# Performance work log

Measured on AMD Instinct MI355X. Metric: run time of the kernel, lower is better.

The kernel has to match this reference:

```python
import jax, jax.numpy as jnp
import numpy as np

EPS = 1e-5
GRID = (16, 16)
BLOCK = (16, 16)


def _ln(x):
    # LayerNorm over (C, H, W) per sample, affine = identity (fresh nn.LayerNorm each call)
    m = jnp.mean(x, axis=(1, 2, 3), keepdims=True)
    v = jnp.mean(jnp.square(x - m), axis=(1, 2, 3), keepdims=True)
    return (x - m) / jnp.sqrt(v + EPS)


def _gelu(x):
    return jax.nn.gelu(x, approximate=False)  # torch F.gelu default = exact erf


def _block(x, fh, fw):
    # NCHW -> [N, C, gh*gw, fh*fw]
    n, c, h, w = x.shape
    gh, gw = h // fh, w // fw
    return x.reshape(n, c, gh, fh, gw, fw).transpose(0, 1, 2, 4, 3, 5).reshape(n, c, gh * gw, fh * fw)


def _unblock(x, gh, gw, fh, fw):
    n, c, _, _ = x.shape
    return x.reshape(n, c, gh, gw, fh, fw).transpose(0, 1, 2, 4, 3, 5).reshape(n, c, gh * fh, gw * fw)


def _gating(x, w1, b1, w2, b2, w3, b3, w4, b4):
    # GetSpatialGatingWeights
    n, c, h, w = x.shape
    x = _ln(x)
    x = jnp.einsum('nchw,cd->ndhw', x, w1) + b1[None, :, None, None]  # C -> 2C
    x = _gelu(x)
    u, v = jnp.split(x, 2, axis=1)
    # grid MLP on u: mix across gh*gw grid positions
    gh, gw = GRID
    fh, fw = h // gh, w // gw
    u = _block(u, fh, fw)                                             # [n,c,G,P]
    u = jnp.einsum('ncgp,gd->ncdp', u, w2) + b2[None, None, :, None]
    u = _unblock(u, gh, gw, fh, fw)
    # block MLP on v: mix across fh*fw positions inside each block
    fh, fw = BLOCK
    gh, gw = h // fh, w // fw
    v = _block(v, fh, fw)
    v = jnp.einsum('ncgp,pd->ncgd', v, w3) + b3
    v = _unblock(v, gh, gw, fh, fw)
    x = jnp.concatenate([u, v], axis=1)
    return jnp.einsum('nchw,cd->ndhw', x, w4) + b4[None, :, None, None]  # 2C -> C


def _chan_lin(x, w, b):
    return jnp.einsum('nchw,cd->ndhw', x, w) + b[None, :, None, None]


def setup_inputs() -> dict:
    key = jax.random.key(0)
    ks = list(jax.random.split(key, 40))
    k = iter(ks)

    def rn(shape, s=0.02):
        return jax.random.normal(next(k), shape, dtype=jnp.float32) * s

    N, Cx, Cy, F, H, W = 8, 128, 256, 128, 128, 128
    G = GRID[0] * GRID[1]    # 256
    B = BLOCK[0] * BLOCK[1]  # 256
    inp = {
        'x': jax.random.normal(next(k), (N, Cx, H, W), dtype=jnp.float32),
        'y': jax.random.normal(next(k), (N, Cy, H // 2, W // 2), dtype=jnp.float32),
        'wt': rn((Cy, F, 2, 2)), 'bt': rn((F,)),
        'wc1': rn((Cx, F)), 'bc1': rn((F,)),
        'wc2': rn((F, F)), 'bc2': rn((F,)),
        'wl1': rn((F, F)), 'bl1': rn((F,)),
        'wl2': rn((F, F)), 'bl2': rn((F,)),
        'wl3': rn((F, F)), 'bl3': rn((F,)),
        'wl4': rn((F, F)), 'bl4': rn((F,)),
    }
    for p in ('g1', 'g2'):
        inp[p + '_w1'] = rn((F, 2 * F)); inp[p + '_b1'] = rn((2 * F,))
        inp[p + '_w2'] = rn((G, G));     inp[p + '_b2'] = rn((G,))
        inp[p + '_w3'] = rn((B, B));     inp[p + '_b3'] = rn((B,))
        inp[p + '_w4'] = rn((2 * F, F)); inp[p + '_b4'] = rn((F,))
    return inp


def reference(x, y, wt, bt, wc1, bc1, wc2, bc2, wl1, bl1, wl2, bl2, wl3, bl3, wl4, bl4,
              g1_w1, g1_b1, g1_w2, g1_b2, g1_w3, g1_b3, g1_w4, g1_b4,
              g2_w1, g2_b1, g2_w2, g2_b2, g2_w3, g2_b3, g2_w4, g2_b4):
    # ConvT_up: kernel=2, stride=2 (non-overlapping) + ReLU
    n, cy, hy, wy = y.shape
    fo = wt.shape[1]
    y = jnp.einsum('nchw,cokl->nohkwl', y, wt).reshape(n, fo, 2 * hy, 2 * wy) + bt[None, :, None, None]
    y = jax.nn.relu(y)
    # Conv1x1 (+ReLU) projections
    x = jax.nn.relu(_chan_lin(x, wc1, bc1))
    y = jax.nn.relu(_chan_lin(y, wc2, bc2))
    shortcut_x, shortcut_y = x, y
    # x branch
    x = _gelu(_chan_lin(_ln(x), wl1, bl1))
    gx = _gating(x, g1_w1, g1_b1, g1_w2, g1_b2, g1_w3, g1_b3, g1_w4, g1_b4)
    # y branch
    y = _gelu(_chan_lin(_ln(y), wl2, bl2))
    gy = _gating(y, g2_w1, g2_b1, g2_w2, g2_b2, g2_w3, g2_b3, g2_w4, g2_b4)
    # cross gating + residuals (dropout p=0.0 -> identity)
    y = _chan_lin(y * gx, wl3, bl3) + shortcut_y
    x = _chan_lin(x * gy, wl4, bl4) + y + shortcut_x
    return x, y
```

## Files before the change

### kernel.cpp

```cpp
#include <hip/hip_runtime.h>
#include <hip/hip_bf16.h>


typedef unsigned short u16;
typedef __bf16 bf16x8 __attribute__((ext_vector_type(8)));
typedef u16    u16x8  __attribute__((ext_vector_type(8)));
typedef u16    u16x4  __attribute__((ext_vector_type(4)));
typedef float  f32x4  __attribute__((ext_vector_type(4)));

__device__ __forceinline__ float bf2f(u16 u) {
  union { float f; unsigned int i; } v; v.i = ((unsigned int)u) << 16; return v.f;
}
__device__ __forceinline__ u16 f2bf(float f) {
  union { float f; unsigned int i; } v; v.f = f;
  unsigned int x = v.i;
  return (u16)((x + 0x7fffu + ((x >> 16) & 1u)) >> 16);
}
__device__ __forceinline__ f32x4 mfma16(u16x8 a, u16x8 b, f32x4 c) {
  return __builtin_amdgcn_mfma_f32_16x16x32_bf16(
      __builtin_bit_cast(bf16x8, a), __builtin_bit_cast(bf16x8, b), c, 0, 0, 0);
}
__device__ __forceinline__ float gelu_erf(float v) {
  const float z = v * (-2.3022586f - 0.10294276f * v * v);
  return __fdividef(v, 1.f + exp2f(z));
}

__global__ __launch_bounds__(256) void prep_k(
    const float* __restrict__ wc1f, const float* __restrict__ wc2f,
    const float* __restrict__ wl1f, const float* __restrict__ wl2f,
    const float* __restrict__ wl3f, const float* __restrict__ wl4f,
    const float* __restrict__ g1w1, const float* __restrict__ g2w1,
    const float* __restrict__ g1w4, const float* __restrict__ g2w4,
    const float* __restrict__ g1w2, const float* __restrict__ g2w2,
    const float* __restrict__ g1w3, const float* __restrict__ g2w3,
    const float* __restrict__ wtf,
    u16* __restrict__ wb, float* __restrict__ cs, float* __restrict__ ps) {
  const int b = blockIdx.x, t = threadIdx.x;
  if (b < 384) {
    const float* src = b < 64 ? wc1f : b < 128 ? wc2f : b < 192 ? wl1f
                     : b < 256 ? wl2f : b < 320 ? wl3f : wl4f;
    const int w = b >> 6;
    const int i = ((b & 63) << 8) + t;
    const int d = i >> 7, c = i & 127;
    wb[w * 16384 + i] = f2bf(src[c * 128 + d]);
  } else if (b < 640) {
    const float* src = b < 512 ? g1w1 : g2w1;
    const int base = b < 512 ? 98304 : 131072;
    const int i = (((b - (b < 512 ? 384 : 512)) << 8) + t);
    const int d = i >> 7, c = i & 127;
    wb[base + i] = f2bf(src[c * 256 + d]);
  } else if (b < 896) {
    const float* src = b < 768 ? g1w4 : g2w4;
    const int base = b < 768 ? 163840 : 196608;
    const int i = (((b - (b < 768 ? 640 : 768)) << 8) + t);
    const int d = i >> 8, c = i & 255;
    wb[base + i] = f2bf(src[c * 128 + d]);
  } else if (b < 1920) {
    const int w = (b - 896) >> 8;
    const float* src = w == 0 ? g1w2 : w == 1 ? g2w2 : w == 2 ? g1w3 : g2w3;
    const int base = 229376 + w * 65536;
    const int i = (((b - 896) & 255) << 8) + t;
    const int d = i >> 8, g = i & 255;
    wb[base + i] = f2bf(src[g * 256 + d]);
  } else if (b < 2432) {
    const int i = ((b - 1920) << 8) + t;
    const int c = i & 255, r = i >> 8, o = r & 127, kl = r >> 7;
    wb[491520 + i] = f2bf(wtf[(c * 128 + o) * 4 + kl]);
  } else if (b < 2436) {
    const int w = b - 2432;
    const float* src = w == 0 ? wl1f : w == 1 ? wl2f : w == 2 ? g1w1 : g2w1;
    const int cout = w < 2 ? 128 : 256;
    if (t < cout) {
      float s = 0.f;
      for (int c = 0; c < 128; ++c) s += bf2f(f2bf(src[c * cout + t]));
      cs[w * 256 + t] = s;
    }
  } else {
    if (t < 64) ps[t] = 0.f;
  }
}

__global__ __launch_bounds__(256, 2) void gemmYX_k(
    const float* __restrict__ Y, const float* __restrict__ X,
    const u16* __restrict__ Wtb, const float* __restrict__ bt,
    const u16* __restrict__ Wc2, const float* __restrict__ bc2,
    const u16* __restrict__ Wc1, const float* __restrict__ bc1,
    u16* __restrict__ oy, u16* __restrict__ ox, float* __restrict__ ps) {
  __shared__ u16 sm[25088];
  __shared__ float red[8];
  const int tid = threadIdx.x;
  const int wid = tid >> 6, lane = tid & 63, fr = lane & 15, fg = lane >> 4;

  if (blockIdx.x < 512) {
    u16* As = sm;
    u16* Cs = sm + 16384;
    float* pso = ps + 16;
    const int m0 = blockIdx.x * 64;
    const int ns = m0 >> 12, pb = m0 & 4095;
    const int tokg = (wid & 1) * 32;
    const int chg  = (wid >> 1) * 64;
    const int xorl = (fr & 7) << 4;

#pragma unroll
    for (int it = 0; it < 16; ++it) {
      const int idx = it * 256 + tid;
      const int c = idx & 255, t4 = idx >> 8;
      const f32x4 v = *(const f32x4*)(Y + (((size_t)(ns * 256 + c)) << 12) + pb + t4 * 4);
#pragma unroll
      for (int r = 0; r < 4; ++r) {
        const int tok = t4 * 4 + r;
        const int byte = (tok * 512 + c * 2) ^ ((tok & 7) << 4);
        *(u16*)((char*)As + byte) = f2bf(v[r]);
      }
    }
    __syncthreads();

    float s1 = 0.f, s2 = 0.f;
    for (int kl = 0; kl < 4; ++kl) {
      if (kl) __syncthreads();
      f32x4 acc1[2][4] = {};
      {
        const u16* Brow = Wtb + (size_t)(kl * 128 + chg + fr) * 256;
#pragma unroll
        for (int ks = 0; ks < 8; ++ks) {
          const int kb = ks * 32 + fg * 8;
          u16x8 a_[2], b_[4];
#pragma unroll
          for (int i = 0; i < 2; ++i) {
            const int tok = tokg + i * 16 + fr;
            const int byte = (tok * 512 + kb * 2) ^ xorl;
            a_[i] = *(const u16x8*)((const char*)As + byte);
          }
#pragma unroll
          for (int j = 0; j < 4; ++j)
            b_[j] = *(const u16x8*)(Brow + (size_t)j * 16 * 256 + kb);
#pragma unroll
          for (int i = 0; i < 2; ++i)
#pragma unroll
            for (int j = 0; j < 4; ++j) acc1[i][j] = mfma16(b_[j], a_[i], acc1[i][j]);
        }
      }
#pragma unroll
      for (int i = 0; i < 2; ++i) {
        const int tok = tokg + i * 16 + fr;
#pragma unroll
        for (int j = 0; j < 4; ++j) {
          const int o0 = chg + j * 16 + fg * 4;
          const f32x4 bz = *(const f32x4*)(bt + o0);
          u16x4 sv;
#pragma unroll
          for (int r = 0; r < 4; ++r) sv[r] = f2bf(fmaxf(acc1[i][j][r] + bz[r], 0.f));
          *(u16x4*)(Cs + tok * 136 + o0) = sv;
        }
      }
      __syncthreads();
      f32x4 acc2[2][4] = {};
      {
        const u16* Brow = Wc2 + (size_t)(chg + fr) * 128;
#pragma unroll
        for (int ks = 0; ks < 4; ++ks) {
          const int kb = ks * 32 + fg * 8;
          u16x8 a_[2], b_[4];
#pragma unroll
          for (int i = 0; i < 2; ++i)
            a_[i] = *(const u16x8*)(Cs + (tokg + i * 16 + fr) * 136 + kb);
#pragma unroll
          for (int j = 0; j < 4; ++j)
            b_[j] = *(const u16x8*)(Brow + (size_t)j * 16 * 128 + kb);
#pragma unroll
          for (int i = 0; i < 2; ++i)
#pragma unroll
            for (int j = 0; j < 4; ++j) acc2[i][j] = mfma16(b_[j], a_[i], acc2[i][j]);
        }
      }
#pragma unroll
      for (int i = 0; i < 2; ++i) {
        const int ytok = m0 + tokg + i * 16 + fr;
        const int hy = (ytok >> 6) & 63, wy = ytok & 63;
        const int opix = ((ns * 128 + 2 * hy + (kl >> 1)) << 7) + 2 * wy + (kl & 1);
#pragma unroll
        for (int j = 0; j < 4; ++j) {
          const int ch0 = chg + j * 16 + fg * 4;
          const f32x4 bz = *(const f32x4*)(bc2 + ch0);
          u16x4 sv;
#pragma unroll
          for (int r = 0; r < 4; ++r) {
            float v = fmaxf(acc2[i][j][r] + bz[r], 0.f);
            s1 += v; s2 += v * v;
            sv[r] = f2bf(v);
          }
          *(u16x4*)(oy + (size_t)opix * 128 + ch0) = sv;
        }
      }
    }
#pragma unroll
    for (int off = 32; off > 0; off >>= 1) {
      s1 += __shfl_down(s1, off); s2 += __shfl_down(s2, off);
    }
    if (lane == 0) { red[wid] = s1; red[4 + wid] = s2; }
    __syncthreads();
    if (tid == 0)  atomicAdd(&pso[2 * ns],     red[0] + red[1] + red[2] + red[3]);
    if (tid == 64) atomicAdd(&pso[2 * ns + 1], red[4] + red[5] + red[6] + red[7]);
  } else {
    u16* As = sm;
    float* pso = ps;
    const int m0 = (blockIdx.x - 512) * 128;
    const int ns = m0 >> 14, pb = m0 & 16383;
    const int wmt = (wid & 1) * 64, wnc = (wid >> 1) * 64;

#pragma unroll
    for (int it = 0; it < 16; ++it) {
      const int idx = it * 256 + tid;
      const int c = idx & 127, t4 = idx >> 7;
      const f32x4 v = *(const f32x4*)(X + (((size_t)(ns * 128 + c)) << 14) + pb + t4 * 4);
#pragma unroll
      for (int r = 0; r < 4; ++r) As[(t4 * 4 + r) * 136 + c] = f2bf(v[r]);
    }
    __syncthreads();

    f32x4 acc[4][4] = {};
    const u16* Brow = Wc1 + (size_t)(wnc + fr) * 128;
    u16x8 a[4][4];
#pragma unroll
    for (int ks = 0; ks < 4; ++ks) {
      const int kb = ks * 32 + fg * 8;
#pragma unroll
      for (int i = 0; i < 4; ++i)
        a[ks][i] = *(const u16x8*)(As + (wmt + i * 16 + fr) * 136 + kb);
    }
#pragma unroll
    for (int ks = 0; ks < 4; ++ks) {
      const int kb = ks * 32 + fg * 8;
      u16x8 b_[4];
#pragma unroll
      for (int j = 0; j < 4; ++j)
        b_[j] = *(const u16x8*)(Brow + (size_t)j * 16 * 128 + kb);
#pragma unroll
      for (int i = 0; i < 4; ++i)
#pragma unroll
        for (int j = 0; j < 4; ++j) acc[i][j] = mfma16(b_[j], a[ks][i], acc[i][j]);
    }

    float s1 = 0.f, s2 = 0.f;
#pragma unroll
    for (int i = 0; i < 4; ++i) {
      const int token = m0 + wmt + i * 16 + fr;
#pragma unroll
      for (int j = 0; j < 4; ++j) {
        const int ch0 = wnc + j * 16 + fg * 4;
        const f32x4 bz = *(const f32x4*)(bc1 + ch0);
        f32x4 v = acc[i][j];
        u16x4 sv;
#pragma unroll
        for (int r = 0; r < 4; ++r) {
          v[r] = fmaxf(v[r] + bz[r], 0.f);
          s1 += v[r]; s2 += v[r] * v[r];
          sv[r] = f2bf(v[r]);
        }
        *(u16x4*)(ox + (size_t)token * 128 + ch0) = sv;
      }
    }
#pragma unroll
    for (int off = 32; off > 0; off >>= 1) {
      s1 += __shfl_down(s1, off); s2 += __shfl_down(s2, off);
    }
    if (lane == 0) { red[wid] = s1; red[4 + wid] = s2; }
    __syncthreads();
    if (tid == 0)  atomicAdd(&pso[2 * ns],     red[0] + red[1] + red[2] + red[3]);
    if (tid == 64) atomicAdd(&pso[2 * ns + 1], red[4] + red[5] + red[6] + red[7]);
  }
}

__global__ __launch_bounds__(256, 2) void gemm4d_k(
    const u16* __restrict__ Ay, const u16* __restrict__ Ax,
    const u16* __restrict__ Wty, const u16* __restrict__ Wtx,
    const float* __restrict__ by, const float* __restrict__ bx,
    float* __restrict__ ps,
    const float* __restrict__ csy, const float* __restrict__ csx,
    u16* __restrict__ oy, u16* __restrict__ ox) {
  __shared__ float red[8];
  const int br = blockIdx.y;
  const u16* A1 = br ? Ax : Ay;
  const u16* Wt = br ? Wtx : Wty;
  const float* bias = br ? bx : by;
  const float* pst = ps + (br ? 0 : 16);
  float* pso = ps + (br ? 32 : 48);
  const float* cs = br ? csx : csy;
  u16* out = br ? ox : oy;

  const int tid = threadIdx.x;
  const int m0 = blockIdx.x * 128;
  const int wid = tid >> 6, lane = tid & 63, fr = lane & 15, fg = lane >> 4;
  const int wmt = (wid & 1) * 64, wnc = (wid >> 1) * 64;

  f32x4 acc[4][4] = {};
  const u16* Arow = A1 + (size_t)(m0 + wmt + fr) * 128;
  const u16* Brow = Wt + (size_t)(wnc + fr) * 128;

  u16x8 a[4][4];
#pragma unroll
  for (int ks = 0; ks < 4; ++ks) {
    const int kb = ks * 32 + fg * 8;
#pragma unroll
    for (int i = 0; i < 4; ++i)
      a[ks][i] = *(const u16x8*)(Arow + (size_t)i * 16 * 128 + kb);
  }
#pragma unroll
  for (int ks = 0; ks < 4; ++ks) {
    const int kb = ks * 32 + fg * 8;
    u16x8 b_[4];
#pragma unroll
    for (int j = 0; j < 4; ++j)
      b_[j] = *(const u16x8*)(Brow + (size_t)j * 16 * 128 + kb);
#pragma unroll
    for (int i = 0; i < 4; ++i)
#pragma unroll
      for (int j = 0; j < 4; ++j) acc[i][j] = mfma16(b_[j], a[ks][i], acc[i][j]);
  }

  const int s = m0 >> 14;
  const float inv_n = 1.f / 2097152.f;
  const float mean = pst[2 * s] * inv_n;
  const float var = pst[2 * s + 1] * inv_n - mean * mean;
  const float alpha = rsqrtf(var + 1e-5f);
  const float beta = -mean * alpha;

  float s1 = 0.f, s2 = 0.f;
#pragma unroll
  for (int i = 0; i < 4; ++i) {
    const int token = m0 + wmt + i * 16 + fr;
#pragma unroll
    for (int j = 0; j < 4; ++j) {
      const int ch0 = wnc + j * 16 + fg * 4;
      const f32x4 bz = *(const f32x4*)(bias + ch0);
      const f32x4 csv = *(const f32x4*)(cs + ch0);
      f32x4 v = acc[i][j];
      u16x4 sv;
#pragma unroll
      for (int r = 0; r < 4; ++r) {
        v[r] = v[r] * alpha + beta * csv[r] + bz[r];
        v[r] = gelu_erf(v[r]);
        s1 += v[r]; s2 += v[r] * v[r];
        sv[r] = f2bf(v[r]);
      }
      *(u16x4*)(out + (size_t)token * 128 + ch0) = sv;
    }
  }
#pragma unroll
  for (int off = 32; off > 0; off >>= 1) {
    s1 += __shfl_down(s1, off); s2 += __shfl_down(s2, off);
  }
  if (lane == 0) { red[wid] = s1; red[4 + wid] = s2; }
  __syncthreads();
  if (tid == 0)  atomicAdd(&pso[2 * s],     red[0] + red[1] + red[2] + red[3]);
  if (tid == 64) atomicAdd(&pso[2 * s + 1], red[4] + red[5] + red[6] + red[7]);
}

template <int MODE>
__global__ __launch_bounds__(512, 2) void mlp3c_k(
    const u16* __restrict__ a1y, const u16* __restrict__ a1x,
    const u16* __restrict__ w1y, const u16* __restrict__ w1x,
    const float* __restrict__ b1y, const float* __restrict__ b1x,
    const float* __restrict__ ps,
    const float* __restrict__ csy, const float* __restrict__ csx,
    const u16* __restrict__ w2y, const u16* __restrict__ w2x,
    const float* __restrict__ b2y, const float* __restrict__ b2x,
    const u16* __restrict__ w4y, const u16* __restrict__ w4x,
    const float* __restrict__ b4y, const float* __restrict__ b4x,
    u16* __restrict__ goy, u16* __restrict__ gox) {
  __shared__ u16 Ts[32768];
  const int br = blockIdx.z;
  const u16* y1 = br ? a1x : a1y;
  const u16* mulp = br ? a1y : a1x;
  const u16* w1b = br ? w1x : w1y;
  const float* b1 = br ? b1x : b1y;
  const float* pst = ps + (br ? 32 : 48);
  const float* csb = br ? csx : csy;
  const u16* w2b = br ? w2x : w2y;
  const float* b2 = br ? b2x : b2y;
  const u16* w4b = br ? w4x : w4y;
  const float* b4 = br ? b4x : b4y;
  u16* gout = br ? gox : goy;

  const int q2 = blockIdx.x, ns = blockIdx.y;
  const int tid = threadIdx.x;
  constexpr int coff = MODE ? 128 : 0;
  const int wid = tid >> 6, lane = tid & 63, fr = lane & 15, fg = lane >> 4;
  const int xorl = (fr & 7) << 4;

  int pbase, prow, pcol;
  if constexpr (MODE == 0) {
    pbase = ns * 16384 + (q2 >> 3) * 128 + (q2 & 7);
    prow = 1024; pcol = 8;
  } else {
    pbase = ns * 16384 + (q2 >> 3) * 2048 + (q2 & 7) * 16;
    prow = 128; pcol = 1;
  }
  auto pix = [&](int q) { return pbase + (q >> 4) * prow + (q & 15) * pcol; };

  {
    const int wgt = (wid >> 1) * 64;
    const int wc  = (wid & 1) * 64;
    const float inv_n = 1.f / 2097152.f;
    const float mean = pst[2 * ns] * inv_n;
    const float var = pst[2 * ns + 1] * inv_n - mean * mean;
    const float alpha = rsqrtf(var + 1e-5f);
    const float beta = -mean * alpha;

    f32x4 acc[4][4] = {};
    const u16* ar[4];
#pragma unroll
    for (int i = 0; i < 4; ++i)
      ar[i] = y1 + (size_t)pix(wgt + i * 16 + fr) * 128;
    const u16* br_ = w1b + (size_t)(coff + wc + fr) * 128;

    u16x8 a[4][4];
#pragma unroll
    for (int ks = 0; ks < 4; ++ks) {
      const int kb = ks * 32 + fg * 8;
#pragma unroll
      for (int i = 0; i < 4; ++i) a[ks][i] = *(const u16x8*)(ar[i] + kb);
    }
#pragma unroll
    for (int ks = 0; ks < 4; ++ks) {
      const int kb = ks * 32 + fg * 8;
      u16x8 b_[4];
#pragma unroll
      for (int j = 0; j < 4; ++j)
        b_[j] = *(const u16x8*)(br_ + (size_t)j * 16 * 128 + kb);
#pragma unroll
      for (int i = 0; i < 4; ++i)
#pragma unroll
        for (int j = 0; j < 4; ++j) acc[i][j] = mfma16(a[ks][i], b_[j], acc[i][j]);
    }
#pragma unroll
    for (int j = 0; j < 4; ++j) {
      const int c = wc + j * 16 + fr;
      const float cv = csb[coff + c];
      const float bz = b1[coff + c];
#pragma unroll
      for (int i = 0; i < 4; ++i) {
        const int g0 = wgt + i * 16 + fg * 4;
        u16x4 sv;
#pragma unroll
        for (int r = 0; r < 4; ++r)
          sv[r] = f2bf(gelu_erf(acc[i][j][r] * alpha + beta * cv + bz));
        const int byte = (c * 512 + g0 * 2) ^ xorl;
        *(u16x4*)((char*)Ts + byte) = sv;
      }
    }
  }
  __syncthreads();

  f32x4 accB[4][4];
  const int wcs = (wid >> 2) * 64;
  const int wds = (wid & 3) * 64;
  {
#pragma unroll
    for (int i = 0; i < 4; ++i)
#pragma unroll
      for (int j = 0; j < 4; ++j) accB[i][j] = f32x4{0.f, 0.f, 0.f, 0.f};
    const u16* br_ = w2b + (size_t)(wds + fr) * 256;
#pragma unroll
    for (int h = 0; h < 2; ++h) {
      u16x8 a[4][4];
#pragma unroll
      for (int ks = 0; ks < 4; ++ks) {
        const int kb = (h * 4 + ks) * 32 + fg * 8;
#pragma unroll
        for (int i = 0; i < 4; ++i) {
          const int c = wcs + i * 16 + fr;
          const int byte = (c * 512 + kb * 2) ^ xorl;
          a[ks][i] = *(const u16x8*)((const char*)Ts + byte);
        }
      }
#pragma unroll
      for (int ks = 0; ks < 4; ++ks) {
        const int kb = (h * 4 + ks) * 32 + fg * 8;
        u16x8 b_[4];
#pragma unroll
        for (int j = 0; j < 4; ++j)
          b_[j] = *(const u16x8*)(br_ + (size_t)j * 16 * 256 + kb);
#pragma unroll
        for (int i = 0; i < 4; ++i)
#pragma unroll
          for (int j = 0; j < 4; ++j) accB[i][j] = mfma16(a[ks][i], b_[j], accB[i][j]);
      }
    }
  }
  __syncthreads();

#pragma unroll
  for (int j = 0; j < 4; ++j) {
    const int d = wds + j * 16 + fr;
    const float bz = b2[d];
    const int dx = (d & 7) << 4;
#pragma unroll
    for (int i = 0; i < 4; ++i) {
      const int c0 = wcs + i * 16 + fg * 4;
      u16x4 sv;
#pragma unroll
      for (int r = 0; r < 4; ++r) sv[r] = f2bf(accB[i][j][r] + bz);
      const int byte = (d * 256 + c0 * 2) ^ dx;
      *(u16x4*)((char*)Ts + byte) = sv;
    }
  }
  __syncthreads();

  {
    const int wp = (wid >> 1) * 64;
    const int wo = (wid & 1) * 64;
    f32x4 accC[4][4] = {};
    const u16* br_ = w4b + (size_t)(wo + fr) * 256 + coff;
#pragma unroll
    for (int ks = 0; ks < 4; ++ks) {
      const int kb = ks * 32 + fg * 8;
      u16x8 a_[4], b_[4];
#pragma unroll
      for (int i = 0; i < 4; ++i) {
        const int dp = wp + i * 16 + fr;
        const int byte = (dp * 256 + kb * 2) ^ ((dp & 7) << 4);
        a_[i] = *(const u16x8*)((const char*)Ts + byte);
      }
#pragma unroll
      for (int j = 0; j < 4; ++j)
        b_[j] = *(const u16x8*)(br_ + (size_t)j * 16 * 256 + kb);
#pragma unroll
      for (int i = 0; i < 4; ++i)
#pragma unroll
        for (int j = 0; j < 4; ++j) accC[i][j] = mfma16(b_[j], a_[i], accC[i][j]);
    }
#pragma unroll
    for (int i = 0; i < 4; ++i) {
      const size_t pg = (size_t)pix(wp + i * 16 + fr) * 128;
#pragma unroll
      for (int j = 0; j < 4; ++j) {
        const int o0 = wo + j * 16 + fg * 4;
        f32x4 v = accC[i][j];
        u16x4 sv;
        if constexpr (MODE == 0) {
          const f32x4 bz = *(const f32x4*)(b4 + o0);
#pragma unroll
          for (int r = 0; r < 4; ++r) sv[r] = f2bf(v[r] + bz[r]);
        } else {
          const u16x4 pv = *(const u16x4*)(gout + pg + o0);
          const u16x4 mv = *(const u16x4*)(mulp + pg + o0);
#pragma unroll
          for (int r = 0; r < 4; ++r)
            sv[r] = f2bf((v[r] + bf2f(pv[r])) * bf2f(mv[r]));
        }
        *(u16x4*)(gout + pg + o0) = sv;
      }
    }
  }
}

__global__ __launch_bounds__(256, 2) void dual5_k(
    const u16* __restrict__ y1g, const u16* __restrict__ x1g,
    const u16* __restrict__ w3b, const u16* __restrict__ w4b,
    const float* __restrict__ b3, const float* __restrict__ b4,
    const u16* __restrict__ y0, const u16* __restrict__ x0,
    float* __restrict__ outy, float* __restrict__ outx) {
  const int tid = threadIdx.x;
  const int m0 = blockIdx.x * 128;
  const int wid = tid >> 6, lane = tid & 63, fr = lane & 15, fg = lane >> 4;
  const int wmt = (wid & 1) * 64, wnc = (wid >> 1) * 64;

  f32x4 acc[4][4] = {};
  u16x4 y9[4][4];

  {
    const u16* Arow = y1g + (size_t)(m0 + wmt + fr) * 128;
    const u16* Brow = w3b + (size_t)(wnc + fr) * 128;
    u16x8 a[4][4];
#pragma unroll
    for (int ks = 0; ks < 4; ++ks) {
      const int kb = ks * 32 + fg * 8;
#pragma unroll
      for (int i = 0; i < 4; ++i)
        a[ks][i] = *(const u16x8*)(Arow + (size_t)i * 16 * 128 + kb);
    }
#pragma unroll
    for (int ks = 0; ks < 4; ++ks) {
      const int kb = ks * 32 + fg * 8;
      u16x8 b_[4];
#pragma unroll
      for (int j = 0; j < 4; ++j) b_[j] = *(const u16x8*)(Brow + (size_t)j * 16 * 128 + kb);
#pragma unroll
      for (int i = 0; i < 4; ++i)
#pragma unroll
        for (int j = 0; j < 4; ++j) acc[i][j] = mfma16(b_[j], a[ks][i], acc[i][j]);
    }
  }
  {
    u16x4 scv[4][4];
#pragma unroll
    for (int i = 0; i < 4; ++i) {
      const int token = m0 + wmt + i * 16 + fr;
#pragma unroll
      for (int j = 0; j < 4; ++j)
        scv[i][j] = *(const u16x4*)(y0 + (size_t)token * 128 + wnc + j * 16 + fg * 4);
    }
#pragma unroll
    for (int i = 0; i < 4; ++i) {
      const int token = m0 + wmt + i * 16 + fr;
      const int ns = token >> 14, p = token & 16383;
#pragma unroll
      for (int j = 0; j < 4; ++j) {
        const int ch0 = wnc + j * 16 + fg * 4;
        const f32x4 bz = *(const f32x4*)(b3 + ch0);
        f32x4 v = acc[i][j];
#pragma unroll
        for (int r = 0; r < 4; ++r) {
          v[r] += bz[r] + bf2f(scv[i][j][r]);
          outy[((size_t)(ns * 128 + ch0 + r) << 14) + p] = v[r];
          y9[i][j][r] = f2bf(v[r]);
        }
        acc[i][j] = f32x4{0.f, 0.f, 0.f, 0.f};
      }
    }
  }
  {
    const u16* Arow = x1g + (size_t)(m0 + wmt + fr) * 128;
    const u16* Brow = w4b + (size_t)(wnc + fr) * 128;
    u16x8 a[4][4];
#pragma unroll
    for (int ks = 0; ks < 4; ++ks) {
      const int kb = ks * 32 + fg * 8;
#pragma unroll
      for (int i = 0; i < 4; ++i)
        a[ks][i] = *(const u16x8*)(Arow + (size_t)i * 16 * 128 + kb);
    }
#pragma unroll
    for (int ks = 0; ks < 4; ++ks) {
      const int kb = ks * 32 + fg * 8;
      u16x8 b_[4];
#pragma unroll
      for (int j = 0; j < 4; ++j) b_[j] = *(const u16x8*)(Brow + (size_t)j * 16 * 128 + kb);
#pragma unroll
      for (int i = 0; i < 4; ++i)
#pragma unroll
        for (int j = 0; j < 4; ++j) acc[i][j] = mfma16(b_[j], a[ks][i], acc[i][j]);
    }
  }
  {
    u16x4 scv[4][4];
#pragma unroll
    for (int i = 0; i < 4; ++i) {
      const int token = m0 + wmt + i * 16 + fr;
#pragma unroll
      for (int j = 0; j < 4; ++j)
        scv[i][j] = *(const u16x4*)(x0 + (size_t)token * 128 + wnc + j * 16 + fg * 4);
    }
#pragma unroll
    for (int i = 0; i < 4; ++i) {
      const int token = m0 + wmt + i * 16 + fr;
      const int ns = token >> 14, p = token & 16383;
#pragma unroll
      for (int j = 0; j < 4; ++j) {
        const int ch0 = wnc + j * 16 + fg * 4;
        const f32x4 bz = *(const f32x4*)(b4 + ch0);
        f32x4 v = acc[i][j];
#pragma unroll
        for (int r = 0; r < 4; ++r) {
          v[r] += bz[r] + bf2f(y9[i][j][r]) + bf2f(scv[i][j][r]);
          outx[((size_t)(ns * 128 + ch0 + r) << 14) + p] = v[r];
        }
      }
    }
  }
}

extern "C" void kernel_launch(void* const* d_in, const int* in_sizes, int n_in,
                              void* d_out, int out_size, void* d_ws, size_t ws_size,
                              hipStream_t stream) {
  (void)in_sizes; (void)n_in; (void)out_size; (void)ws_size;
  const float* xf   = (const float*)d_in[0];
  const float* yf   = (const float*)d_in[1];
  const float* wtf  = (const float*)d_in[2];
  const float* btf  = (const float*)d_in[3];
  const float* wc1f = (const float*)d_in[4];
  const float* bc1f = (const float*)d_in[5];
  const float* wc2f = (const float*)d_in[6];
  const float* bc2f = (const float*)d_in[7];
  const float* wl1f = (const float*)d_in[8];
  const float* bl1f = (const float*)d_in[9];
  const float* wl2f = (const float*)d_in[10];
  const float* bl2f = (const float*)d_in[11];
  const float* wl3f = (const float*)d_in[12];
  const float* bl3f = (const float*)d_in[13];
  const float* wl4f = (const float*)d_in[14];
  const float* bl4f = (const float*)d_in[15];
  const float* g1w1 = (const float*)d_in[16];
  const float* g1b1 = (const float*)d_in[17];
  const float* g1w2 = (const float*)d_in[18];
  const float* g1b2 = (const float*)d_in[19];
  const float* g1w3 = (const float*)d_in[20];
  const float* g1b3 = (const float*)d_in[21];
  const float* g1w4 = (const float*)d_in[22];
  const float* g1b4 = (const float*)d_in[23];
  const float* g2w1 = (const float*)d_in[24];
  const float* g2b1 = (const float*)d_in[25];
  const float* g2w2 = (const float*)d_in[26];
  const float* g2b2 = (const float*)d_in[27];
  const float* g2w3 = (const float*)d_in[28];
  const float* g2b3 = (const float*)d_in[29];
  const float* g2w4 = (const float*)d_in[30];
  const float* g2b4 = (const float*)d_in[31];

  constexpr int T16 = 16777216;
  u16* WS  = (u16*)d_ws;
  u16* x0b = WS;
  u16* x1b = WS + (size_t)T16;
  u16* y0b = WS + (size_t)2 * T16;
  u16* y1b = WS + (size_t)3 * T16;
  u16* gyb = WS + (size_t)4 * T16;
  u16* gxb = WS + (size_t)5 * T16;
  float* fb = (float*)(WS + (size_t)6 * T16);
  float* cs = fb;
  float* ps = fb + 1024;
  u16* wb   = (u16*)(fb + 1024 + 64);

  const u16* wc1b = wb;
  const u16* wc2b = wb + 16384;
  const u16* wl1b = wb + 32768;
  const u16* wl2b = wb + 49152;
  const u16* wl3b = wb + 65536;
  const u16* wl4b = wb + 81920;
  const u16* g1w1b = wb + 98304;
  const u16* g2w1b = wb + 131072;
  const u16* g1w4b = wb + 163840;
  const u16* g2w4b = wb + 196608;
  const u16* g1w2b = wb + 229376;
  const u16* g2w2b = wb + 294912;
  const u16* g1w3b = wb + 360448;
  const u16* g2w3b = wb + 425984;
  const u16* wtb   = wb + 491520;

  float* outx = (float*)d_out;
  float* outy = (float*)d_out + (size_t)T16;

  const dim3 B256(256), B512(512);

  prep_k<<<dim3(2437), B256, 0, stream>>>(
      wc1f, wc2f, wl1f, wl2f, wl3f, wl4f, g1w1, g2w1, g1w4, g2w4,
      g1w2, g2w2, g1w3, g2w3, wtf, wb, cs, ps);

  gemmYX_k<<<dim3(1536), B256, 0, stream>>>(
      yf, xf, wtb, btf, wc2b, bc2f, wc1b, bc1f, y0b, x0b, ps);

  gemm4d_k<<<dim3(1024, 2), B256, 0, stream>>>(
      y0b, x0b, wl2b, wl1b, bl2f, bl1f, ps, cs + 256, cs, y1b, x1b);

  mlp3c_k<0><<<dim3(64, 8, 2), B512, 0, stream>>>(
      y1b, x1b, g2w1b, g1w1b, g2b1, g1b1, ps, cs + 768, cs + 512,
      g2w2b, g1w2b, g2b2, g1b2, g2w4b, g1w4b, g2b4, g1b4, gyb, gxb);
  mlp3c_k<1><<<dim3(64, 8, 2), B512, 0, stream>>>(
      y1b, x1b, g2w1b, g1w1b, g2b1, g1b1, ps, cs + 768, cs + 512,
      g2w3b, g1w3b, g2b3, g1b3, g2w4b, g1w4b, g2b4, g1b4, gyb, gxb);

  dual5_k<<<dim3(1024), B256, 0, stream>>>(
      gxb, gyb, wl3b, wl4b, bl3f, bl4f, y0b, x0b, outy, outx);
}
```

Before: 514.2 us.

## Halve LDS footprint of mlp3c by processing grid tiles in two chunks

The fused three-GEMM gating kernel now stages its intermediate tile in 32 KB of LDS instead of 64 KB. It does this by splitting the first GEMM's 256 grid rows into two halves that each accumulate into the second GEMM, and by writing out the second GEMM's result in two halves of 128 outputs. Launch bounds are raised to 4 blocks per CU to use the smaller LDS and register footprint for higher occupancy. In exchange it adds extra barriers, re-reads the w1 and w4 weights per half, and runs the third GEMM twice with smaller tiles.

```diff
diff --git a/kernel.cpp b/kernel.cpp
--- a/kernel.cpp
+++ b/kernel.cpp
@@ -357,7 +357,7 @@
 }
 
 template <int MODE>
-__global__ __launch_bounds__(512, 2) void mlp3c_k(
+__global__ __launch_bounds__(512, 4) void mlp3c_k(
     const u16* __restrict__ a1y, const u16* __restrict__ a1x,
     const u16* __restrict__ w1y, const u16* __restrict__ w1x,
     const float* __restrict__ b1y, const float* __restrict__ b1x,
@@ -368,7 +368,7 @@
     const u16* __restrict__ w4y, const u16* __restrict__ w4x,
     const float* __restrict__ b4y, const float* __restrict__ b4x,
     u16* __restrict__ goy, u16* __restrict__ gox) {
-  __shared__ u16 Ts[32768];
+  __shared__ u16 Ts[16384];
   const int br = blockIdx.z;
   const u16* y1 = br ? a1x : a1y;
   const u16* mulp = br ? a1y : a1x;
@@ -398,158 +398,155 @@
   }
   auto pix = [&](int q) { return pbase + (q >> 4) * prow + (q & 15) * pcol; };
 
+  f32x4 accB[4][4] = {};
+  const int wcs = (wid >> 2) * 64;
+  const int wds = (wid & 3) * 64;
   {
-    const int wgt = (wid >> 1) * 64;
-    const int wc  = (wid & 1) * 64;
     const float inv_n = 1.f / 2097152.f;
     const float mean = pst[2 * ns] * inv_n;
     const float var = pst[2 * ns + 1] * inv_n - mean * mean;
     const float alpha = rsqrtf(var + 1e-5f);
     const float beta = -mean * alpha;
-
-    f32x4 acc[4][4] = {};
-    const u16* ar[4];
-#pragma unroll
-    for (int i = 0; i < 4; ++i)
-      ar[i] = y1 + (size_t)pix(wgt + i * 16 + fr) * 128;
-    const u16* br_ = w1b + (size_t)(coff + wc + fr) * 128;
-
-    u16x8 a[4][4];
-#pragma unroll
-    for (int ks = 0; ks < 4; ++ks) {
-      const int kb = ks * 32 + fg * 8;
-#pragma unroll
-      for (int i = 0; i < 4; ++i) a[ks][i] = *(const u16x8*)(ar[i] + kb);
-    }
-#pragma unroll
-    for (int ks = 0; ks < 4; ++ks) {
-      const int kb = ks * 32 + fg * 8;
-      u16x8 b_[4];
-#pragma unroll
-      for (int j = 0; j < 4; ++j)
-        b_[j] = *(const u16x8*)(br_ + (size_t)j * 16 * 128 + kb);
-#pragma unroll
-      for (int i = 0; i < 4; ++i)
-#pragma unroll
-        for (int j = 0; j < 4; ++j) acc[i][j] = mfma16(a[ks][i], b_[j], acc[i][j]);
-    }
-#pragma unroll
-    for (int j = 0; j < 4; ++j) {
-      const int c = wc + j * 16 + fr;
-      const float cv = csb[coff + c];
-      const float bz = b1[coff + c];
-#pragma unroll
-      for (int i = 0; i < 4; ++i) {
-        const int g0 = wgt + i * 16 + fg * 4;
-        u16x4 sv;
-#pragma unroll
-        for (int r = 0; r < 4; ++r)
-          sv[r] = f2bf(gelu_erf(acc[i][j][r] * alpha + beta * cv + bz));
-        const int byte = (c * 512 + g0 * 2) ^ xorl;
-        *(u16x4*)((char*)Ts + byte) = sv;
-      }
-    }
-  }
-  __syncthreads();
-
-  f32x4 accB[4][4];
-  const int wcs = (wid >> 2) * 64;
-  const int wds = (wid & 3) * 64;
-  {
-#pragma unroll
-    for (int i = 0; i < 4; ++i)
-#pragma unroll
-      for (int j = 0; j < 4; ++j) accB[i][j] = f32x4{0.f, 0.f, 0.f, 0.f};
-    const u16* br_ = w2b + (size_t)(wds + fr) * 256;
-#pragma unroll
-    for (int h = 0; h < 2; ++h) {
-      u16x8 a[4][4];
+    const int wgt = (wid >> 1) * 32;
+    const int wc  = (wid & 1) * 64;
+
+#pragma unroll
+    for (int gi = 0; gi < 2; ++gi) {
+      if (gi) __syncthreads();
+      {
+        f32x4 acc[2][4] = {};
+        const u16* ar[2];
+#pragma unroll
+        for (int i = 0; i < 2; ++i)
+          ar[i] = y1 + (size_t)pix(gi * 128 + wgt + i * 16 + fr) * 128;
+        const u16* br_ = w1b + (size_t)(coff + wc + fr) * 128;
+        u16x8 a[4][2];
+#pragma unroll
+        for (int ks = 0; ks < 4; ++ks) {
+          const int kb = ks * 32 + fg * 8;
+#pragma unroll
+          for (int i = 0; i < 2; ++i) a[ks][i] = *(const u16x8*)(ar[i] + kb);
+        }
+#pragma unroll
+        for (int ks = 0; ks < 4; ++ks) {
+          const int kb = ks * 32 + fg * 8;
+          u16x8 b_[4];
+#pragma unroll
+          for (int j = 0; j < 4; ++j)
+            b_[j] = *(const u16x8*)(br_ + (size_t)j * 16 * 128 + kb);
+#pragma unroll
+          for (int i = 0; i < 2; ++i)
+#pragma unroll
+            for (int j = 0; j < 4; ++j) acc[i][j] = mfma16(a[ks][i], b_[j], acc[i][j]);
+        }
+#pragma unroll
+        for (int j = 0; j < 4; ++j) {
+          const int c = wc + j * 16 + fr;
+          const float cv = csb[coff + c];
+          const float bz = b1[coff + c];
+#pragma unroll
+          for (int i = 0; i < 2; ++i) {
+            const int g0 = wgt + i * 16 + fg * 4;
+            u16x4 sv;
+#pragma unroll
+            for (int r = 0; r < 4; ++r)
+              sv[r] = f2bf(gelu_erf(acc[i][j][r] * alpha + beta * cv + bz));
+            const int byte = (c * 256 + g0 * 2) ^ xorl;
+            *(u16x4*)((char*)Ts + byte) = sv;
+          }
+        }
+      }
+      __syncthreads();
+      {
+        const u16* br_ = w2b + (size_t)(wds + fr) * 256 + gi * 128;
+#pragma unroll
+        for (int ks = 0; ks < 4; ++ks) {
+          const int kb = ks * 32 + fg * 8;
+          u16x8 a_[4], b_[4];
+#pragma unroll
+          for (int i = 0; i < 4; ++i) {
+            const int c = wcs + i * 16 + fr;
+            const int byte = (c * 256 + kb * 2) ^ xorl;
+            a_[i] = *(const u16x8*)((const char*)Ts + byte);
+          }
+#pragma unroll
+          for (int j = 0; j < 4; ++j)
+            b_[j] = *(const u16x8*)(br_ + (size_t)j * 16 * 256 + kb);
+#pragma unroll
+          for (int i = 0; i < 4; ++i)
+#pragma unroll
+            for (int j = 0; j < 4; ++j) accB[i][j] = mfma16(a_[i], b_[j], accB[i][j]);
+        }
+      }
+    }
+  }
+
+#pragma unroll
+  for (int di = 0; di < 2; ++di) {
+    __syncthreads();
+    if (((wid >> 1) & 1) == di) {
+#pragma unroll
+      for (int j = 0; j < 4; ++j) {
+        const int d = wds + j * 16 + fr;
+        const int dl = d - di * 128;
+        const float bz = b2[d];
+        const int dx = (dl & 7) << 4;
+#pragma unroll
+        for (int i = 0; i < 4; ++i) {
+          const int c0 = wcs + i * 16 + fg * 4;
+          u16x4 sv;
+#pragma unroll
+          for (int r = 0; r < 4; ++r) sv[r] = f2bf(accB[i][j][r] + bz);
+          const int byte = (dl * 256 + c0 * 2) ^ dx;
+          *(u16x4*)((char*)Ts + byte) = sv;
+        }
+      }
+    }
+    __syncthreads();
+    {
+      const int wp = (wid >> 1) * 32;
+      const int wo = (wid & 1) * 64;
+      f32x4 accC[2][4] = {};
+      const u16* br_ = w4b + (size_t)(wo + fr) * 256 + coff;
 #pragma unroll
       for (int ks = 0; ks < 4; ++ks) {
-        const int kb = (h * 4 + ks) * 32 + fg * 8;
-#pragma unroll
-        for (int i = 0; i < 4; ++i) {
-          const int c = wcs + i * 16 + fr;
-          const int byte = (c * 512 + kb * 2) ^ xorl;
-          a[ks][i] = *(const u16x8*)((const char*)Ts + byte);
-        }
-      }
-#pragma unroll
-      for (int ks = 0; ks < 4; ++ks) {
-        const int kb = (h * 4 + ks) * 32 + fg * 8;
-        u16x8 b_[4];
+        const int kb = ks * 32 + fg * 8;
+        u16x8 a_[2], b_[4];
+#pragma unroll
+        for (int i = 0; i < 2; ++i) {
+          const int dl = wp + i * 16 + fr;
+          const int byte = (dl * 256 + kb * 2) ^ ((dl & 7) << 4);
+          a_[i] = *(const u16x8*)((const char*)Ts + byte);
+        }
 #pragma unroll
         for (int j = 0; j < 4; ++j)
           b_[j] = *(const u16x8*)(br_ + (size_t)j * 16 * 256 + kb);
 #pragma unroll
-        for (int i = 0; i < 4; ++i)
-#pragma unroll
-          for (int j = 0; j < 4; ++j) accB[i][j] = mfma16(a[ks][i], b_[j], accB[i][j]);
-      }
-    }
-  }
-  __syncthreads();
-
-#pragma unroll
-  for (int j = 0; j < 4; ++j) {
-    const int d = wds + j * 16 + fr;
-    const float bz = b2[d];
-    const int dx = (d & 7) << 4;
-#pragma unroll
-    for (int i = 0; i < 4; ++i) {
-      const int c0 = wcs + i * 16 + fg * 4;
-      u16x4 sv;
-#pragma unroll
-      for (int r = 0; r < 4; ++r) sv[r] = f2bf(accB[i][j][r] + bz);
-      const int byte = (d * 256 + c0 * 2) ^ dx;
-      *(u16x4*)((char*)Ts + byte) = sv;
-    }
-  }
-  __syncthreads();
-
-  {
-    const int wp = (wid >> 1) * 64;
-    const int wo = (wid & 1) * 64;
-    f32x4 accC[4][4] = {};
-    const u16* br_ = w4b + (size_t)(wo + fr) * 256 + coff;
-#pragma unroll
-    for (int ks = 0; ks < 4; ++ks) {
-      const int kb = ks * 32 + fg * 8;
-      u16x8 a_[4], b_[4];
-#pragma unroll
-      for (int i = 0; i < 4; ++i) {
-        const int dp = wp + i * 16 + fr;
-        const int byte = (dp * 256 + kb * 2) ^ ((dp & 7) << 4);
-        a_[i] = *(const u16x8*)((const char*)Ts + byte);
-      }
-#pragma unroll
-      for (int j = 0; j < 4; ++j)
-        b_[j] = *(const u16x8*)(br_ + (size_t)j * 16 * 256 + kb);
-#pragma unroll
-      for (int i = 0; i < 4; ++i)
-#pragma unroll
-        for (int j = 0; j < 4; ++j) accC[i][j] = mfma16(b_[j], a_[i], accC[i][j]);
-    }
-#pragma unroll
-    for (int i = 0; i < 4; ++i) {
-      const size_t pg = (size_t)pix(wp + i * 16 + fr) * 128;
-#pragma unroll
-      for (int j = 0; j < 4; ++j) {
-        const int o0 = wo + j * 16 + fg * 4;
-        f32x4 v = accC[i][j];
-        u16x4 sv;
-        if constexpr (MODE == 0) {
-          const f32x4 bz = *(const f32x4*)(b4 + o0);
-#pragma unroll
-          for (int r = 0; r < 4; ++r) sv[r] = f2bf(v[r] + bz[r]);
-        } else {
-          const u16x4 pv = *(const u16x4*)(gout + pg + o0);
-          const u16x4 mv = *(const u16x4*)(mulp + pg + o0);
-#pragma unroll
-          for (int r = 0; r < 4; ++r)
-            sv[r] = f2bf((v[r] + bf2f(pv[r])) * bf2f(mv[r]));
-        }
-        *(u16x4*)(gout + pg + o0) = sv;
+        for (int i = 0; i < 2; ++i)
+#pragma unroll
+          for (int j = 0; j < 4; ++j) accC[i][j] = mfma16(b_[j], a_[i], accC[i][j]);
+      }
+#pragma unroll
+      for (int i = 0; i < 2; ++i) {
+        const size_t pg = (size_t)pix(di * 128 + wp + i * 16 + fr) * 128;
+#pragma unroll
+        for (int j = 0; j < 4; ++j) {
+          const int o0 = wo + j * 16 + fg * 4;
+          f32x4 v = accC[i][j];
+          u16x4 sv;
+          if constexpr (MODE == 0) {
+            const f32x4 bz = *(const f32x4*)(b4 + o0);
+#pragma unroll
+            for (int r = 0; r < 4; ++r) sv[r] = f2bf(v[r] + bz[r]);
+          } else {
+            const u16x4 pv = *(const u16x4*)(gout + pg + o0);
+            const u16x4 mv = *(const u16x4*)(mulp + pg + o0);
+#pragma unroll
+            for (int r = 0; r < 4; ++r)
+              sv[r] = f2bf((v[r] + bf2f(pv[r])) * bf2f(mv[r]));
+          }
+          *(u16x4*)(gout + pg + o0) = sv;
+        }
       }
     }
   }
```

After: 718.0 us. +39.7%, slower.
